# Performance work log

Measured on AMD Instinct MI355X. Metric: run time of the kernel, lower is better.

Reference implementation:

```python
import jax, jax.numpy as jnp
import numpy as np

D = 768
B = 32
N = 768


def setup_inputs() -> dict:
    key = jax.random.key(0)
    k1, k2, k3, k4 = jax.random.split(key, 4)
    stdv = 1.0 / np.sqrt(D)
    X = jax.random.normal(k1, (B, N, D), dtype=jnp.float32)
    adj = jax.random.uniform(k2, (B, N, N), dtype=jnp.float32)
    W_l = jax.random.uniform(k3, (D, D), dtype=jnp.float32, minval=-stdv, maxval=stdv)
    W_l1 = jax.random.uniform(k4, (D, D), dtype=jnp.float32, minval=-stdv, maxval=stdv)
    return {"X": X, "adj": adj, "W_l": W_l, "W_l1": W_l1}


def _row_normalize(adj):
    # rowsum^-1 with inf -> 0 (rows summing to zero stay zero)
    rowsum = adj.sum(axis=-1, keepdims=True)  # [B, N, 1]
    r_inv = jnp.where(rowsum == 0, 0.0, 1.0 / rowsum)
    return adj * r_inv


def reference(X, adj, W_l, W_l1):
    # X: [B, N, D], adj: [B, N, N]
    adj_n = _row_normalize(adj)
    e1 = jnp.einsum('bnd,de->bne', X, W_l1)        # message transform
    e11 = jnp.einsum('bnm,bmd->bnd', adj_n, e1)    # aggregate
    X1 = jnp.einsum('bnd,de->bne', X, W_l)         # self transform
    h = X1 + e11
    return jax.nn.leaky_relu(h, negative_slope=0.01)
```

## Files before the change

### kernel.cpp

```cpp
#include <hip/hip_runtime.h>
#include <hip/hip_bf16.h>
#include <cstdint>
#include <cstddef>

#define BN_ROWS 24576
#define DD 768
#define BE (768*768)
#define BM 384
#define BN_T 192
#define BK 64

typedef __attribute__((ext_vector_type(8))) short bf16x8;
typedef __attribute__((ext_vector_type(4))) float f32x4;

static __device__ __forceinline__ unsigned short f2bf(float f) {
  unsigned int u = __builtin_bit_cast(unsigned int, f);
  unsigned int lsb = (u >> 16) & 1u;
  u += 0x7fffu + lsb;
  return (unsigned short)(u >> 16);
}


__global__ __launch_bounds__(256) void convertX(const float* __restrict__ x,
                                                unsigned short* __restrict__ xb, int n4) {
  int idx = blockIdx.x * blockDim.x + threadIdx.x;
  int stride = gridDim.x * blockDim.x;
  for (int i = idx; i < n4; i += stride) {
    float4 v = reinterpret_cast<const float4*>(x)[i];
    ushort4 o;
    o.x = f2bf(v.x); o.y = f2bf(v.y); o.z = f2bf(v.z); o.w = f2bf(v.w);
    reinterpret_cast<ushort4*>(xb)[i] = o;
  }
}

__global__ __launch_bounds__(256) void convertWT(const float* __restrict__ Wl,
                                                 const float* __restrict__ Wl1,
                                                 unsigned short* __restrict__ WlT,
                                                 unsigned short* __restrict__ Wl1T) {
  int tid = blockIdx.x * blockDim.x + threadIdx.x;
  if (tid < BE) {
    int d = tid / DD, e = tid % DD;
    WlT[e * DD + d]  = f2bf(Wl[tid]);
    Wl1T[e * DD + d] = f2bf(Wl1[tid]);
  }
}

__global__ __launch_bounds__(256) void adjNorm(const float* __restrict__ adj,
                                               unsigned short* __restrict__ adjnb) {
  int wid = threadIdx.x >> 6, lane = threadIdx.x & 63;
  int row = blockIdx.x * 4 + wid;
  const float4* a = reinterpret_cast<const float4*>(adj + (size_t)row * DD);
  float4 v[3];
  float s = 0.f;
  #pragma unroll
  for (int i = 0; i < 3; ++i) {
    v[i] = a[i * 64 + lane];
    s += (v[i].x + v[i].y) + (v[i].z + v[i].w);
  }
  #pragma unroll
  for (int off = 32; off; off >>= 1) s += __shfl_down(s, off);
  s = __shfl(s, 0);
  float rinv = (s == 0.f) ? 0.f : 1.f / s;
  ushort4* o = reinterpret_cast<ushort4*>(adjnb + (size_t)row * DD);
  #pragma unroll
  for (int i = 0; i < 3; ++i) {
    ushort4 u;
    u.x = f2bf(v[i].x * rinv); u.y = f2bf(v[i].y * rinv);
    u.z = f2bf(v[i].z * rinv); u.w = f2bf(v[i].w * rinv);
    o[i * 64 + lane] = u;
  }
}


template<int MODE>
__global__ __launch_bounds__(512, 2) void gemm8(
    const unsigned short* __restrict__ P0,
    const unsigned short* __restrict__ P1,
    const unsigned short* __restrict__ P2,
    const unsigned short* __restrict__ P3,
    void* __restrict__ outp)
{
  __shared__ char smem[147456];
  constexpr int NT = MODE ? 24 : 12;
  const int tid = threadIdx.x, lane = tid & 63;
  const int wid = tid >> 6, wr = wid >> 1, wc = wid & 1;

  const int logical = (blockIdx.x & 7) * 32 + (blockIdx.x >> 3);

  const unsigned short *Ab0, *Bb0, *Ab1 = nullptr, *Bb1 = nullptr;
  int mt, nt, b;
  if (MODE == 0) {
    mt = logical >> 2; nt = logical & 3;
    b = mt >> 1;
    Ab0 = P0 + (size_t)mt * BM * DD;
    Bb0 = P1 + (size_t)nt * BN_T * DD;
  } else {
    b = logical >> 3; int r = logical & 7; mt = r >> 2; nt = r & 3;
    size_t bo = (size_t)b * BE;
    Ab0 = P0 + bo + (size_t)mt * BM * DD;
    Bb0 = P1 + bo + (size_t)nt * BN_T * DD;
    Ab1 = P2 + bo + (size_t)mt * BM * DD;
    Bb1 = P3 + (size_t)nt * BN_T * DD;
  }

  const int srow = tid >> 3;
  const int sslot = (tid & 7) ^ (srow & 7);
  const int lane_off = srow * DD + sslot * 8;
  const int wchunk = (tid >> 6) * 1024;

  auto stage = [&](int s, int g) {
    int sc = s < NT ? s : 0;
    const unsigned short* base;
    int kk;
    if (MODE == 1 && sc >= 12) { kk = sc - 12; base = (g == 2) ? Bb1 : Ab1; }
    else                       { kk = sc;      base = (g == 2) ? Bb0 : Ab0; }
    const unsigned short* p = base + (size_t)(g == 1 ? 192 : 0) * DD + kk * BK + lane_off;
    char* dst = smem + ((g == 2) ? (98304 + (s & 1) * 24576)
                                 : ((s & 1) * 49152 + g * 24576)) + wchunk;
    #pragma unroll
    for (int i = 0; i < 3; ++i) {
      __builtin_amdgcn_global_load_lds(
          (const __attribute__((address_space(1))) void*)(p + (size_t)i * 64 * DD),
          (__attribute__((address_space(3))) void*)(dst + i * 8192), 16, 0, 0);
    }
  };

  auto frag = [&](int bufbase, int rowbase, int ks) -> bf16x8 {
    int row = rowbase + (lane & 15);
    int slot = (ks * 4 + (lane >> 4)) ^ (row & 7);
    return *reinterpret_cast<const bf16x8*>(smem + bufbase + row * 128 + slot * 16);
  };

  f32x4 acc[6][6] = {};
  bf16x8 a0[3][2], a1[3][2], bb[3][2];

  stage(0, 0); stage(0, 1); stage(0, 2); stage(1, 0);
  asm volatile("s_waitcnt vmcnt(3)" ::: "memory");
  __builtin_amdgcn_s_barrier();

  for (int t = 0; t < NT; ++t) {
    const int Ab = (t & 1) * 49152;
    const int Bb = 98304 + (t & 1) * 24576;

    #pragma unroll
    for (int i = 0; i < 3; ++i) {
      a0[i][0] = frag(Ab, wr * 96 + i * 16, 0);
      a0[i][1] = frag(Ab, wr * 96 + i * 16, 1);
      bb[i][0] = frag(Bb, wc * 96 + i * 16, 0);
      bb[i][1] = frag(Bb, wc * 96 + i * 16, 1);
    }
    stage(t + 1, 1);
    __builtin_amdgcn_s_barrier();
    __builtin_amdgcn_s_setprio(1);
    #pragma unroll
    for (int ks = 0; ks < 2; ++ks)
      #pragma unroll
      for (int mi = 0; mi < 3; ++mi)
        #pragma unroll
        for (int ni = 0; ni < 3; ++ni)
          acc[mi][ni] = __builtin_amdgcn_mfma_f32_16x16x32_bf16(a0[mi][ks], bb[ni][ks], acc[mi][ni], 0, 0, 0);
    __builtin_amdgcn_s_setprio(0);
    __builtin_amdgcn_s_barrier();

    #pragma unroll
    for (int i = 0; i < 3; ++i) {
      a1[i][0] = frag(Ab, wr * 96 + 48 + i * 16, 0);
      a1[i][1] = frag(Ab, wr * 96 + 48 + i * 16, 1);
    }
    stage(t + 1, 2);
    __builtin_amdgcn_s_barrier();
    __builtin_amdgcn_s_setprio(1);
    #pragma unroll
    for (int ks = 0; ks < 2; ++ks)
      #pragma unroll
      for (int mi = 0; mi < 3; ++mi)
        #pragma unroll
        for (int ni = 0; ni < 3; ++ni)
          acc[3 + mi][ni] = __builtin_amdgcn_mfma_f32_16x16x32_bf16(a1[mi][ks], bb[ni][ks], acc[3 + mi][ni], 0, 0, 0);
    __builtin_amdgcn_s_setprio(0);
    __builtin_amdgcn_s_barrier();

    #pragma unroll
    for (int i = 0; i < 3; ++i) {
      bb[i][0] = frag(Bb, wc * 96 + 48 + i * 16, 0);
      bb[i][1] = frag(Bb, wc * 96 + 48 + i * 16, 1);
    }
    __builtin_amdgcn_s_barrier();
    __builtin_amdgcn_s_setprio(1);
    #pragma unroll
    for (int ks = 0; ks < 2; ++ks)
      #pragma unroll
      for (int mi = 0; mi < 3; ++mi)
        #pragma unroll
        for (int ni = 0; ni < 3; ++ni)
          acc[3 + mi][3 + ni] = __builtin_amdgcn_mfma_f32_16x16x32_bf16(a1[mi][ks], bb[ni][ks], acc[3 + mi][3 + ni], 0, 0, 0);
    __builtin_amdgcn_s_setprio(0);
    __builtin_amdgcn_s_barrier();

    stage(t + 2, 0);
    __builtin_amdgcn_s_barrier();
    __builtin_amdgcn_s_setprio(1);
    #pragma unroll
    for (int ks = 0; ks < 2; ++ks)
      #pragma unroll
      for (int mi = 0; mi < 3; ++mi)
        #pragma unroll
        for (int ni = 0; ni < 3; ++ni)
          acc[mi][3 + ni] = __builtin_amdgcn_mfma_f32_16x16x32_bf16(a0[mi][ks], bb[ni][ks], acc[mi][3 + ni], 0, 0, 0);
    __builtin_amdgcn_s_setprio(0);
    asm volatile("s_waitcnt vmcnt(3)" ::: "memory");
    __builtin_amdgcn_s_barrier();
  }

  if (MODE == 0) {
    unsigned short* ob = (unsigned short*)outp + (size_t)b * BE;
    const int mloc = (mt & 1) * BM + wr * 96 + (lane >> 4) * 4;
    #pragma unroll
    for (int mi = 0; mi < 6; ++mi)
      #pragma unroll
      for (int ni = 0; ni < 6; ++ni) {
        int m = mloc + mi * 16;
        int d = nt * BN_T + wc * 96 + ni * 16 + (lane & 15);
        f32x4 v = acc[mi][ni];
        ushort4 o;
        o.x = f2bf(v[0]); o.y = f2bf(v[1]); o.z = f2bf(v[2]); o.w = f2bf(v[3]);
        *reinterpret_cast<ushort4*>(ob + (size_t)d * DD + m) = o;
      }
  } else {
    float* ob = (float*)outp + (size_t)b * BE;
    const int mloc = mt * BM + wr * 96 + (lane >> 4) * 4;
    #pragma unroll
    for (int mi = 0; mi < 6; ++mi)
      #pragma unroll
      for (int ni = 0; ni < 6; ++ni) {
        int m = mloc + mi * 16;
        int n = nt * BN_T + wc * 96 + ni * 16 + (lane & 15);
        f32x4 v = acc[mi][ni];
        #pragma unroll
        for (int j = 0; j < 4; ++j) {
          float x = v[j];
          ob[(size_t)(m + j) * DD + n] = x > 0.f ? x : 0.01f * x;
        }
      }
  }
}


extern "C" void kernel_launch(void* const* d_in, const int* in_sizes, int n_in,
                              void* d_out, int out_size, void* d_ws, size_t ws_size,
                              hipStream_t stream) {
  const float* X   = (const float*)d_in[0];
  const float* adj = (const float*)d_in[1];
  const float* Wl  = (const float*)d_in[2];
  const float* Wl1 = (const float*)d_in[3];
  float* out = (float*)d_out;

  char* ws = (char*)d_ws;
  const size_t SZ = (size_t)BN_ROWS * DD * 2;
  unsigned short* Xb    = (unsigned short*)(ws);
  unsigned short* adjnb = (unsigned short*)(ws + SZ);
  unsigned short* e1T   = (unsigned short*)(ws + 2 * SZ);
  unsigned short* WlT   = (unsigned short*)(ws + 3 * SZ);
  unsigned short* Wl1T  = (unsigned short*)(ws + 3 * SZ + (size_t)BE * 2);

  convertX<<<4096, 256, 0, stream>>>(X, Xb, (BN_ROWS * DD) / 4);
  convertWT<<<(BE + 255) / 256, 256, 0, stream>>>(Wl, Wl1, WlT, Wl1T);
  adjNorm<<<BN_ROWS / 4, 256, 0, stream>>>(adj, adjnb);
  gemm8<0><<<256, 512, 0, stream>>>(Xb, Wl1T, nullptr, nullptr, e1T);
  gemm8<1><<<256, 512, 0, stream>>>(adjnb, e1T, Xb, WlT, out);
}
```

Measured before the change: 161.4 us.

## Replace four-phase interleaved pipeline with two-phase k-split loop and full-tile prefetch

```diff
diff --git a/kernel.cpp b/kernel.cpp
--- a/kernel.cpp
+++ b/kernel.cpp
@@ -132,10 +132,10 @@
   };
 
   f32x4 acc[6][6] = {};
-  bf16x8 a0[3][2], a1[3][2], bb[3][2];
-
-  stage(0, 0); stage(0, 1); stage(0, 2); stage(1, 0);
-  asm volatile("s_waitcnt vmcnt(3)" ::: "memory");
+  bf16x8 af[6], bf[6];
+
+  stage(0, 0); stage(0, 1); stage(0, 2);
+  asm volatile("s_waitcnt vmcnt(0)" ::: "memory");
   __builtin_amdgcn_s_barrier();
 
   for (int t = 0; t < NT; ++t) {
@@ -143,72 +143,35 @@
     const int Bb = 98304 + (t & 1) * 24576;
 
     #pragma unroll
-    for (int i = 0; i < 3; ++i) {
-      a0[i][0] = frag(Ab, wr * 96 + i * 16, 0);
-      a0[i][1] = frag(Ab, wr * 96 + i * 16, 1);
-      bb[i][0] = frag(Bb, wc * 96 + i * 16, 0);
-      bb[i][1] = frag(Bb, wc * 96 + i * 16, 1);
+    for (int i = 0; i < 6; ++i) {
+      af[i] = frag(Ab, wr * 96 + i * 16, 0);
+      bf[i] = frag(Bb, wc * 96 + i * 16, 0);
     }
-    stage(t + 1, 1);
+    stage(t + 1, 0); stage(t + 1, 1); stage(t + 1, 2);
     __builtin_amdgcn_s_barrier();
     __builtin_amdgcn_s_setprio(1);
     #pragma unroll
-    for (int ks = 0; ks < 2; ++ks)
-      #pragma unroll
-      for (int mi = 0; mi < 3; ++mi)
-        #pragma unroll
-        for (int ni = 0; ni < 3; ++ni)
-          acc[mi][ni] = __builtin_amdgcn_mfma_f32_16x16x32_bf16(a0[mi][ks], bb[ni][ks], acc[mi][ni], 0, 0, 0);
+    for (int mi = 0; mi < 6; ++mi)
+      #pragma unroll
+      for (int ni = 0; ni < 6; ++ni)
+        acc[mi][ni] = __builtin_amdgcn_mfma_f32_16x16x32_bf16(af[mi], bf[ni], acc[mi][ni], 0, 0, 0);
     __builtin_amdgcn_s_setprio(0);
     __builtin_amdgcn_s_barrier();
 
     #pragma unroll
-    for (int i = 0; i < 3; ++i) {
-      a1[i][0] = frag(Ab, wr * 96 + 48 + i * 16, 0);
-      a1[i][1] = frag(Ab, wr * 96 + 48 + i * 16, 1);
+    for (int i = 0; i < 6; ++i) {
+      af[i] = frag(Ab, wr * 96 + i * 16, 1);
+      bf[i] = frag(Bb, wc * 96 + i * 16, 1);
     }
-    stage(t + 1, 2);
     __builtin_amdgcn_s_barrier();
     __builtin_amdgcn_s_setprio(1);
     #pragma unroll
-    for (int ks = 0; ks < 2; ++ks)
-      #pragma unroll
-      for (int mi = 0; mi < 3; ++mi)
-        #pragma unroll
-        for (int ni = 0; ni < 3; ++ni)
-          acc[3 + mi][ni] = __builtin_amdgcn_mfma_f32_16x16x32_bf16(a1[mi][ks], bb[ni][ks], acc[3 + mi][ni], 0, 0, 0);
+    for (int mi = 0; mi < 6; ++mi)
+      #pragma unroll
+      for (int ni = 0; ni < 6; ++ni)
+        acc[mi][ni] = __builtin_amdgcn_mfma_f32_16x16x32_bf16(af[mi], bf[ni], acc[mi][ni], 0, 0, 0);
     __builtin_amdgcn_s_setprio(0);
-    __builtin_amdgcn_s_barrier();
-
-    #pragma unroll
-    for (int i = 0; i < 3; ++i) {
-      bb[i][0] = frag(Bb, wc * 96 + 48 + i * 16, 0);
-      bb[i][1] = frag(Bb, wc * 96 + 48 + i * 16, 1);
-    }
-    __builtin_amdgcn_s_barrier();
-    __builtin_amdgcn_s_setprio(1);
-    #pragma unroll
-    for (int ks = 0; ks < 2; ++ks)
-      #pragma unroll
-      for (int mi = 0; mi < 3; ++mi)
-        #pragma unroll
-        for (int ni = 0; ni < 3; ++ni)
-          acc[3 + mi][3 + ni] = __builtin_amdgcn_mfma_f32_16x16x32_bf16(a1[mi][ks], bb[ni][ks], acc[3 + mi][3 + ni], 0, 0, 0);
-    __builtin_amdgcn_s_setprio(0);
-    __builtin_amdgcn_s_barrier();
-
-    stage(t + 2, 0);
-    __builtin_amdgcn_s_barrier();
-    __builtin_amdgcn_s_setprio(1);
-    #pragma unroll
-    for (int ks = 0; ks < 2; ++ks)
-      #pragma unroll
-      for (int mi = 0; mi < 3; ++mi)
-        #pragma unroll
-        for (int ni = 0; ni < 3; ++ni)
-          acc[mi][3 + ni] = __builtin_amdgcn_mfma_f32_16x16x32_bf16(a0[mi][ks], bb[ni][ks], acc[mi][3 + ni], 0, 0, 0);
-    __builtin_amdgcn_s_setprio(0);
-    asm volatile("s_waitcnt vmcnt(3)" ::: "memory");
+    asm volatile("s_waitcnt vmcnt(0)" ::: "memory");
     __builtin_amdgcn_s_barrier();
   }
 
```

Result: faster. 154.5 us (-4.2%).
